# Kernel optimization log

Measured on AMD Instinct MI355X. Metric: run time of the kernel, lower is better.

## Reference

```python
import jax, jax.numpy as jnp
import numpy as np

N_NODES = 50000
N_EDGES = 1600000
N_GRAPHS = 256
IN_CH = 128
HID = 128
OUT_CH = 10


def gcn_conv(x, W, b, src, dst, ew, num_nodes):
    # PyG GCNConv: add self-loops (weight 1), symmetric deg^-1/2 normalization,
    # linear transform first, aggregate via scatter-add, bias after.
    loop = jnp.arange(num_nodes)
    s = jnp.concatenate([src, loop])
    d = jnp.concatenate([dst, loop])
    w = jnp.concatenate([ew, jnp.ones((num_nodes,), x.dtype)])
    deg = jax.ops.segment_sum(w, d, num_segments=num_nodes)
    dinv = jnp.where(deg > 0, jax.lax.rsqrt(deg), 0.0)
    norm = dinv[s] * dinv[d] * w                     # [E+N]
    h = x @ W                                        # [N, H]
    msg = h[s] * norm[:, None]                       # gather + scale
    out = jax.ops.segment_sum(msg, d, num_segments=num_nodes)  # scatter-add
    return out + b


def setup_inputs() -> dict:
    key = jax.random.key(0)
    ks = jax.random.split(key, 12)
    x = jax.random.normal(ks[0], (N_NODES, IN_CH), jnp.float32)
    edge_index = jax.random.randint(ks[1], (2, N_EDGES), 0, N_NODES, jnp.int64)
    edge_weight = jax.random.uniform(ks[2], (N_EDGES,), jnp.float32)
    batch = jnp.sort(jax.random.randint(ks[3], (N_NODES,), 0, N_GRAPHS, jnp.int64))
    s = 1.0 / np.sqrt(HID)
    W1 = jax.random.normal(ks[4], (IN_CH, HID), jnp.float32) / np.sqrt(IN_CH)
    b1 = jnp.zeros((HID,), jnp.float32)
    W2 = jax.random.normal(ks[5], (HID, HID), jnp.float32) * s
    b2 = jnp.zeros((HID,), jnp.float32)
    W3 = jax.random.normal(ks[6], (HID, HID), jnp.float32) * s
    b3 = jnp.zeros((HID,), jnp.float32)
    lw1 = jax.random.normal(ks[7], (HID, HID), jnp.float32) * s
    lb1 = jax.random.normal(ks[8], (HID,), jnp.float32) * s
    lw2 = jax.random.normal(ks[9], (HID, OUT_CH), jnp.float32) * s
    lb2 = jax.random.normal(ks[10], (OUT_CH,), jnp.float32) * s
    return {"x": x, "edge_index": edge_index, "edge_weight": edge_weight,
            "batch": batch, "W1": W1, "b1": b1, "W2": W2, "b2": b2,
            "W3": W3, "b3": b3, "lw1": lw1, "lb1": lb1, "lw2": lw2, "lb2": lb2}


def reference(x, edge_index, edge_weight, batch, W1, b1, W2, b2, W3, b3, lw1, lb1, lw2, lb2):
    src, dst = edge_index[0], edge_index[1]
    h = jax.nn.relu(gcn_conv(x, W1, b1, src, dst, edge_weight, N_NODES))
    h = jax.nn.relu(gcn_conv(h, W2, b2, src, dst, edge_weight, N_NODES))
    h = gcn_conv(h, W3, b3, src, dst, edge_weight, N_NODES)
    # global mean pool over graphs
    sums = jax.ops.segment_sum(h, batch, num_segments=N_GRAPHS)
    cnt = jax.ops.segment_sum(jnp.ones((N_NODES,), h.dtype), batch, num_segments=N_GRAPHS)
    emb = sums / jnp.maximum(cnt, 1.0)[:, None]      # [G, HID]
    out = (emb @ lw1 + lb1) @ lw2 + lb2              # classify: lin1 -> lin2
    return out
```

## Files before the change

### kernel.cpp

```cpp
#include <hip/hip_runtime.h>

#define N_NODES 50000
#define N_EDGES 1600000
#define N_GRAPHS 256
#define HID 128
#define OUT_CH 10
#define PAD 80
#define NBUCK 512
#define BNODES ((N_NODES + NBUCK - 1) / NBUCK)
#define BCAP 6144
#define P1BLK 256
#define EPB (N_EDGES / P1BLK)
#define DSENTINEL 127

typedef __bf16 bf16x8 __attribute__((ext_vector_type(8)));
typedef float f32x4 __attribute__((ext_vector_type(4)));

__device__ inline unsigned bf16rne(float f) {
    unsigned u = __float_as_uint(f);
    return (u + 0x7fffu + ((u >> 16) & 1u)) >> 16;
}

__global__ __launch_bounds__(1024) void bucket_k(const int* __restrict__ src,
                                                 const int* __restrict__ dst,
                                                 const float* __restrict__ ew,
                                                 int* __restrict__ bcount,
                                                 int2* __restrict__ cpair) {
    __shared__ int hist[NBUCK];
    __shared__ int base[NBUCK];
    int t = threadIdx.x;
    for (int i = t; i < NBUCK; i += 1024) hist[i] = 0;
    __syncthreads();
    int e0 = blockIdx.x * EPB;
    int e1 = e0 + EPB;
    for (int e = e0 + t; e < e1; e += 1024)
        atomicAdd(&hist[dst[e] / BNODES], 1);
    __syncthreads();
    for (int i = t; i < NBUCK; i += 1024) {
        int c = hist[i];
        base[i] = (c > 0) ? atomicAdd(&bcount[i], (c + 7) & ~7) : 0;
        hist[i] = 0;
    }
    __syncthreads();
    for (int e = e0 + t; e < e1; e += 1024) {
        int d = dst[e];
        int b = d / BNODES;
        int off = base[b] + atomicAdd(&hist[b], 1);
        if (off < BCAP) {
            int2 p;
            p.x = ((d - b * BNODES) << 16) | src[e];
            p.y = __float_as_int(ew[e]);
            cpair[b * BCAP + off] = p;
        }
    }
    __syncthreads();
    for (int i = t; i < NBUCK; i += 1024) {
        int c = hist[i];
        int ac = (c + 7) & ~7;
        for (int j = c; j < ac; ++j) {
            int off = base[i] + j;
            if (off < BCAP) {
                int2 p;
                p.x = DSENTINEL << 16;
                p.y = 0;
                cpair[i * BCAP + off] = p;
            }
        }
    }
}

__global__ __launch_bounds__(512) void ell_scatter_k(const int* __restrict__ bcount,
                                                     const int2* __restrict__ cpair,
                                                     int2* __restrict__ ell,
                                                     int* __restrict__ fill,
                                                     float* __restrict__ dinv) {
    __shared__ int lfill[BNODES];
    __shared__ float wsum[BNODES];
    int b = blockIdx.x;
    int t = threadIdx.x;
    for (int i = t; i < BNODES; i += 512) {
        lfill[i] = 0;
        wsum[i] = 0.f;
    }
    __syncthreads();
    int cnt = bcount[b];
    if (cnt > BCAP) cnt = BCAP;
    int n0 = b * BNODES;
    int sbase = b * BCAP;
    for (int i = t; i < cnt; i += 512) {
        int2 p = cpair[sbase + i];
        int dloc = p.x >> 16;
        if (dloc < BNODES) {
            int pos = atomicAdd(&lfill[dloc], 1);
            atomicAdd(&wsum[dloc], __int_as_float(p.y));
            if (pos < PAD) {
                int2 q;
                q.x = p.x & 0xffff;
                q.y = p.y;
                ell[(size_t)(n0 + dloc) * PAD + pos] = q;
            }
        }
    }
    __syncthreads();
    for (int i = t; i < BNODES; i += 512) {
        int n = n0 + i;
        if (n < N_NODES) {
            fill[n] = lfill[i] < PAD ? lfill[i] : PAD;
            dinv[n] = rsqrtf(wsum[i] + 1.0f);
        }
    }
}

__global__ __launch_bounds__(256) void scale_k(int2* __restrict__ ell,
                                               const int* __restrict__ fill,
                                               const float* __restrict__ dinv) {
    int idx = blockIdx.x * blockDim.x + threadIdx.x;
    if (idx >= N_NODES * PAD) return;
    int n = idx / PAD;
    int j = idx - n * PAD;
    if (j < fill[n]) {
        int2 p = ell[idx];
        p.y = __float_as_int(__int_as_float(p.y) * dinv[p.x] * dinv[n]);
        ell[idx] = p;
    }
}

__global__ void wprep_k(const float* __restrict__ W1, const float* __restrict__ W2,
                        const float* __restrict__ W3, unsigned short* __restrict__ Wt) {
    int idx = blockIdx.x * 256 + threadIdx.x;
    if (idx >= 3 * 16384) return;
    int m = idx >> 14;
    int r = idx & 16383;
    const float* W = (m == 0) ? W1 : (m == 1) ? W2 : W3;
    int c = r >> 7, k = r & 127;
    Wt[idx] = (unsigned short)bf16rne(W[k * 128 + c]);
}

__global__ __launch_bounds__(256) void gemm_mfma_k(const float* __restrict__ A32,
                                                   const unsigned short* __restrict__ Ab,
                                                   const unsigned short* __restrict__ Wt,
                                                   unsigned short* __restrict__ Cb,
                                                   int n_rows) {
    int tid = threadIdx.x;
    int wave = tid >> 6;
    int lane = tid & 63;
    int m = lane & 15;
    int quad = lane >> 4;
    int row = blockIdx.x * 64 + wave * 16 + m;
    int rowc = row < n_rows ? row : n_rows - 1;
    f32x4 acc[8] = {};
#pragma unroll
    for (int kc = 0; kc < 4; ++kc) {
        bf16x8 a;
        if (A32) {
            const float4* Ar = (const float4*)(A32 + (size_t)rowc * 128 + kc * 32 + quad * 8);
            float4 lo = Ar[0], hi = Ar[1];
            union { bf16x8 v; unsigned short s[8]; } u;
            u.s[0] = (unsigned short)bf16rne(lo.x);
            u.s[1] = (unsigned short)bf16rne(lo.y);
            u.s[2] = (unsigned short)bf16rne(lo.z);
            u.s[3] = (unsigned short)bf16rne(lo.w);
            u.s[4] = (unsigned short)bf16rne(hi.x);
            u.s[5] = (unsigned short)bf16rne(hi.y);
            u.s[6] = (unsigned short)bf16rne(hi.z);
            u.s[7] = (unsigned short)bf16rne(hi.w);
            a = u.v;
        } else {
            a = *(const bf16x8*)(Ab + (size_t)rowc * 128 + kc * 32 + quad * 8);
        }
#pragma unroll
        for (int ct = 0; ct < 8; ++ct) {
            bf16x8 b = *(const bf16x8*)(Wt + (size_t)(ct * 16 + m) * 128 + kc * 32 + quad * 8);
            acc[ct] = __builtin_amdgcn_mfma_f32_16x16x32_bf16(a, b, acc[ct], 0, 0, 0);
        }
    }
    int obase = blockIdx.x * 64 + wave * 16 + quad * 4;
#pragma unroll
    for (int ct = 0; ct < 8; ++ct) {
#pragma unroll
        for (int r = 0; r < 4; ++r) {
            int n = obase + r;
            if (n < n_rows)
                Cb[(size_t)n * 128 + ct * 16 + m] = (unsigned short)bf16rne(acc[ct][r]);
        }
    }
}

__global__ __launch_bounds__(256) void agg_k(const unsigned short* __restrict__ tb,
                                             const int* __restrict__ fill,
                                             const int2* __restrict__ ell,
                                             const float* __restrict__ dinv,
                                             const float* __restrict__ bias,
                                             unsigned short* __restrict__ outB, int relu) {
    int lane = threadIdx.x & 31;
    int local = threadIdx.x >> 5;
    int n = blockIdx.x * 8 + local;
    if (n >= N_NODES) return;
    float di = dinv[n];
    float sw = di * di;
#define BF4(q, f0, f1, f2, f3)                                    \
    float f0 = __uint_as_float((q).x << 16);                      \
    float f1 = __uint_as_float((q).x & 0xffff0000u);              \
    float f2 = __uint_as_float((q).y << 16);                      \
    float f3 = __uint_as_float((q).y & 0xffff0000u);
    uint2 qs = ((const uint2*)(tb + (size_t)n * 128))[lane];
    BF4(qs, sx, sy, sz, sw4)
    float4 acc = make_float4(sx * sw, sy * sw, sz * sw, sw4 * sw);
    const int2* ep = ell + n * PAD;
    int c = fill[n];
    int i = 0;
    for (; i + 8 <= c; i += 8) {
        int2 p0 = ep[i], p1 = ep[i + 1], p2 = ep[i + 2], p3 = ep[i + 3];
        int2 p4 = ep[i + 4], p5 = ep[i + 5], p6 = ep[i + 6], p7 = ep[i + 7];
        uint2 q0 = ((const uint2*)(tb + (size_t)p0.x * 128))[lane];
        uint2 q1 = ((const uint2*)(tb + (size_t)p1.x * 128))[lane];
        uint2 q2 = ((const uint2*)(tb + (size_t)p2.x * 128))[lane];
        uint2 q3 = ((const uint2*)(tb + (size_t)p3.x * 128))[lane];
        uint2 q4 = ((const uint2*)(tb + (size_t)p4.x * 128))[lane];
        uint2 q5 = ((const uint2*)(tb + (size_t)p5.x * 128))[lane];
        uint2 q6 = ((const uint2*)(tb + (size_t)p6.x * 128))[lane];
        uint2 q7 = ((const uint2*)(tb + (size_t)p7.x * 128))[lane];
        float w0 = __int_as_float(p0.y), w1 = __int_as_float(p1.y);
        float w2 = __int_as_float(p2.y), w3 = __int_as_float(p3.y);
        float w4 = __int_as_float(p4.y), w5 = __int_as_float(p5.y);
        float w6 = __int_as_float(p6.y), w7 = __int_as_float(p7.y);
        BF4(q0, a0, b0, c0, d0)
        BF4(q1, a1, b1, c1, d1)
        BF4(q2, a2, b2, c2, d2)
        BF4(q3, a3, b3, c3, d3)
        BF4(q4, a4, b4, c4, d4)
        BF4(q5, a5, b5, c5, d5)
        BF4(q6, a6, b6, c6, d6)
        BF4(q7, a7, b7, c7, d7)
        acc.x += a0 * w0 + a1 * w1 + a2 * w2 + a3 * w3 + a4 * w4 + a5 * w5 + a6 * w6 + a7 * w7;
        acc.y += b0 * w0 + b1 * w1 + b2 * w2 + b3 * w3 + b4 * w4 + b5 * w5 + b6 * w6 + b7 * w7;
        acc.z += c0 * w0 + c1 * w1 + c2 * w2 + c3 * w3 + c4 * w4 + c5 * w5 + c6 * w6 + c7 * w7;
        acc.w += d0 * w0 + d1 * w1 + d2 * w2 + d3 * w3 + d4 * w4 + d5 * w5 + d6 * w6 + d7 * w7;
    }
    for (; i + 4 <= c; i += 4) {
        int2 p0 = ep[i], p1 = ep[i + 1], p2 = ep[i + 2], p3 = ep[i + 3];
        float w0 = __int_as_float(p0.y), w1 = __int_as_float(p1.y);
        float w2 = __int_as_float(p2.y), w3 = __int_as_float(p3.y);
        uint2 q0 = ((const uint2*)(tb + (size_t)p0.x * 128))[lane];
        uint2 q1 = ((const uint2*)(tb + (size_t)p1.x * 128))[lane];
        uint2 q2 = ((const uint2*)(tb + (size_t)p2.x * 128))[lane];
        uint2 q3 = ((const uint2*)(tb + (size_t)p3.x * 128))[lane];
        BF4(q0, a0, b0, c0, d0)
        BF4(q1, a1, b1, c1, d1)
        BF4(q2, a2, b2, c2, d2)
        BF4(q3, a3, b3, c3, d3)
        acc.x += a0 * w0 + a1 * w1 + a2 * w2 + a3 * w3;
        acc.y += b0 * w0 + b1 * w1 + b2 * w2 + b3 * w3;
        acc.z += c0 * w0 + c1 * w1 + c2 * w2 + c3 * w3;
        acc.w += d0 * w0 + d1 * w1 + d2 * w2 + d3 * w3;
    }
    for (; i < c; ++i) {
        int2 p = ep[i];
        float w = __int_as_float(p.y);
        uint2 q = ((const uint2*)(tb + (size_t)p.x * 128))[lane];
        BF4(q, a0, b0, c0, d0)
        acc.x += a0 * w; acc.y += b0 * w; acc.z += c0 * w; acc.w += d0 * w;
    }
#undef BF4
    float4 b = ((const float4*)bias)[lane];
    acc.x += b.x; acc.y += b.y; acc.z += b.z; acc.w += b.w;
    if (relu) {
        acc.x = fmaxf(acc.x, 0.f);
        acc.y = fmaxf(acc.y, 0.f);
        acc.z = fmaxf(acc.z, 0.f);
        acc.w = fmaxf(acc.w, 0.f);
    }
    uint2 pk;
    pk.x = bf16rne(acc.x) | (bf16rne(acc.y) << 16);
    pk.y = bf16rne(acc.z) | (bf16rne(acc.w) << 16);
    ((uint2*)(outB + (size_t)n * 128))[lane] = pk;
}

__global__ void gbound_k(const int* __restrict__ batch, int* __restrict__ gstart) {
    int n = blockIdx.x * blockDim.x + threadIdx.x;
    if (n >= N_NODES) return;
    int b = batch[n];
    int bprev = (n == 0) ? -1 : batch[n - 1];
    for (int g = bprev + 1; g <= b; ++g) gstart[g] = n;
    if (n == N_NODES - 1) {
        for (int g = b + 1; g <= N_GRAPHS; ++g) gstart[g] = N_NODES;
    }
}

#define PCHUNK 49
__global__ __launch_bounds__(128) void pool1_k(const unsigned short* __restrict__ hb,
                                               const int* __restrict__ batch,
                                               float* __restrict__ pool) {
    int c = threadIdx.x;
    int n0 = blockIdx.x * PCHUNK;
    if (n0 >= N_NODES) return;
    int n1 = n0 + PCHUNK;
    if (n1 > N_NODES) n1 = N_NODES;
    int g = batch[n0];
    float run = 0.f;
    for (int n = n0; n < n1; ++n) {
        int gn = batch[n];
        if (gn != g) {
            atomicAdd(&pool[g * 128 + c], run);
            run = 0.f;
            g = gn;
        }
        run += __uint_as_float((unsigned)hb[(size_t)n * 128 + c] << 16);
    }
    atomicAdd(&pool[g * 128 + c], run);
}

__global__ __launch_bounds__(128) void cls2_k(const float* __restrict__ pool,
                                              const int* __restrict__ gstart,
                                              const float* __restrict__ lw1,
                                              const float* __restrict__ lb1,
                                              const float* __restrict__ lw2,
                                              const float* __restrict__ lb2,
                                              float* __restrict__ out) {
    __shared__ float emb[128];
    __shared__ float mid[128];
    int g = blockIdx.x, c = threadIdx.x;
    float cntf = fmaxf((float)(gstart[g + 1] - gstart[g]), 1.0f);
    emb[c] = pool[(size_t)g * 128 + c] / cntf;
    __syncthreads();
    float a = lb1[c];
    for (int k = 0; k < 128; ++k) a += emb[k] * lw1[k * 128 + c];
    mid[c] = a;
    __syncthreads();
    if (c < OUT_CH) {
        float o = lb2[c];
        for (int k = 0; k < 128; ++k) o += mid[k] * lw2[k * OUT_CH + c];
        out[g * OUT_CH + c] = o;
    }
}

extern "C" void kernel_launch(void* const* d_in, const int* in_sizes, int n_in,
                              void* d_out, int out_size, void* d_ws, size_t ws_size,
                              hipStream_t stream) {
    const float* x = (const float*)d_in[0];
    const int* ei = (const int*)d_in[1];
    const int* src = ei;
    const int* dst = ei + N_EDGES;
    const float* ew = (const float*)d_in[2];
    const int* batch = (const int*)d_in[3];
    const float* W1 = (const float*)d_in[4];
    const float* b1 = (const float*)d_in[5];
    const float* W2 = (const float*)d_in[6];
    const float* b2 = (const float*)d_in[7];
    const float* W3 = (const float*)d_in[8];
    const float* b3 = (const float*)d_in[9];
    const float* lw1 = (const float*)d_in[10];
    const float* lb1 = (const float*)d_in[11];
    const float* lw2 = (const float*)d_in[12];
    const float* lb2 = (const float*)d_in[13];
    float* out = (float*)d_out;

    char* ws = (char*)d_ws;
    size_t off = 0;
    auto alloc = [&](size_t bytes) {
        size_t cur = off;
        off += (bytes + 255) & ~(size_t)255;
        return cur;
    };
    size_t o_bcount = alloc(NBUCK * 4);
    size_t o_pool = alloc(N_GRAPHS * HID * 4);
    size_t zero_end = off;
    size_t o_fill = alloc(N_NODES * 4);
    size_t o_dinv = alloc(N_NODES * 4);
    size_t o_gstart = alloc((N_GRAPHS + 1) * 4);
    size_t o_wt = alloc(3 * 16384 * 2);
    size_t o_ell = alloc((size_t)N_NODES * PAD * 8);
    size_t o_cpair = alloc((size_t)NBUCK * BCAP * 8);
    size_t o_gAb = alloc((size_t)N_NODES * HID * 2);
    size_t o_aggB = alloc((size_t)N_NODES * HID * 2);
    (void)ws_size;

    int* bcount = (int*)(ws + o_bcount);
    float* pool = (float*)(ws + o_pool);
    int* fill = (int*)(ws + o_fill);
    float* dinv = (float*)(ws + o_dinv);
    int* gstart = (int*)(ws + o_gstart);
    unsigned short* Wt = (unsigned short*)(ws + o_wt);
    int2* ell = (int2*)(ws + o_ell);
    int2* cpair = (int2*)(ws + o_cpair);
    unsigned short* gAb = (unsigned short*)(ws + o_gAb);
    unsigned short* aggB = (unsigned short*)(ws + o_aggB);

    hipMemsetAsync(d_ws, 0, zero_end, stream);

    int nb = (N_NODES + 255) / 256;
    bucket_k<<<P1BLK, 1024, 0, stream>>>(src, dst, ew, bcount, cpair);
    ell_scatter_k<<<NBUCK, 512, 0, stream>>>(bcount, cpair, ell, fill, dinv);
    scale_k<<<(N_NODES * PAD + 255) / 256, 256, 0, stream>>>(ell, fill, dinv);
    gbound_k<<<nb, 256, 0, stream>>>(batch, gstart);
    wprep_k<<<192, 256, 0, stream>>>(W1, W2, W3, Wt);

    int gemm_blocks = (N_NODES + 63) / 64;
    int agg_blocks = (N_NODES + 7) / 8;
    gemm_mfma_k<<<gemm_blocks, 256, 0, stream>>>(x, (const unsigned short*)0, Wt, gAb, N_NODES);
    agg_k<<<agg_blocks, 256, 0, stream>>>(gAb, fill, ell, dinv, b1, aggB, 1);
    gemm_mfma_k<<<gemm_blocks, 256, 0, stream>>>((const float*)0, aggB, Wt + 16384, gAb, N_NODES);
    agg_k<<<agg_blocks, 256, 0, stream>>>(gAb, fill, ell, dinv, b2, aggB, 1);
    gemm_mfma_k<<<gemm_blocks, 256, 0, stream>>>((const float*)0, aggB, Wt + 32768, gAb, N_NODES);
    agg_k<<<agg_blocks, 256, 0, stream>>>(gAb, fill, ell, dinv, b3, aggB, 0);

    pool1_k<<<(N_NODES + PCHUNK - 1) / PCHUNK, 128, 0, stream>>>(aggB, batch, pool);
    cls2_k<<<N_GRAPHS, 128, 0, stream>>>(pool, gstart, lw1, lb1, lw2, lb2, out);
}
```

Baseline: 400.0 us.

## Widen aggregation gathers to 16 lanes per node, vectorize bucketing, fuse prep kernels

The aggregation kernel now gives each node 16 lanes, each loading a uint4 (8 bf16 features), instead of 32 lanes loading uint2. That doubles the nodes per block and reduces the number of memory instructions per gathered row. The bucketing kernel reads dst as int4 with 250 blocks so each block's edge range stays int4-aligned. The gbound and weight-prep kernels are merged into one launch. The aggregation unroll drops from 8 to 4 neighbors, which may reduce memory-level parallelism per thread.

```diff
diff --git a/kernel.cpp b/kernel.cpp
--- a/kernel.cpp
+++ b/kernel.cpp
@@ -9,7 +9,7 @@
 #define NBUCK 512
 #define BNODES ((N_NODES + NBUCK - 1) / NBUCK)
 #define BCAP 6144
-#define P1BLK 256
+#define P1BLK 250
 #define EPB (N_EDGES / P1BLK)
 #define DSENTINEL 127
 
@@ -31,10 +31,16 @@
     int t = threadIdx.x;
     for (int i = t; i < NBUCK; i += 1024) hist[i] = 0;
     __syncthreads();
-    int e0 = blockIdx.x * EPB;
-    int e1 = e0 + EPB;
-    for (int e = e0 + t; e < e1; e += 1024)
-        atomicAdd(&hist[dst[e] / BNODES], 1);
+    const int ch0 = blockIdx.x * (EPB / 4);
+    const int ch1 = ch0 + (EPB / 4);
+    const int4* dst4 = (const int4*)dst;
+    for (int ci = ch0 + t; ci < ch1; ci += 1024) {
+        int4 d4 = dst4[ci];
+        atomicAdd(&hist[d4.x / BNODES], 1);
+        atomicAdd(&hist[d4.y / BNODES], 1);
+        atomicAdd(&hist[d4.z / BNODES], 1);
+        atomicAdd(&hist[d4.w / BNODES], 1);
+    }
     __syncthreads();
     for (int i = t; i < NBUCK; i += 1024) {
         int c = hist[i];
@@ -42,16 +48,25 @@
         hist[i] = 0;
     }
     __syncthreads();
-    for (int e = e0 + t; e < e1; e += 1024) {
-        int d = dst[e];
-        int b = d / BNODES;
-        int off = base[b] + atomicAdd(&hist[b], 1);
-        if (off < BCAP) {
-            int2 p;
-            p.x = ((d - b * BNODES) << 16) | src[e];
-            p.y = __float_as_int(ew[e]);
-            cpair[b * BCAP + off] = p;
-        }
+    for (int ci = ch0 + t; ci < ch1; ci += 1024) {
+        int4 d4 = dst4[ci];
+        int e = ci * 4;
+#define PROC(dd, ee)                                              \
+        {                                                         \
+            int b = (dd) / BNODES;                                \
+            int off = base[b] + atomicAdd(&hist[b], 1);           \
+            if (off < BCAP) {                                     \
+                int2 p;                                           \
+                p.x = (((dd) - b * BNODES) << 16) | src[ee];      \
+                p.y = __float_as_int(ew[ee]);                     \
+                cpair[b * BCAP + off] = p;                        \
+            }                                                     \
+        }
+        PROC(d4.x, e)
+        PROC(d4.y, e + 1)
+        PROC(d4.z, e + 2)
+        PROC(d4.w, e + 3)
+#undef PROC
     }
     __syncthreads();
     for (int i = t; i < NBUCK; i += 1024) {
@@ -125,15 +140,28 @@
     }
 }
 
-__global__ void wprep_k(const float* __restrict__ W1, const float* __restrict__ W2,
-                        const float* __restrict__ W3, unsigned short* __restrict__ Wt) {
+__global__ __launch_bounds__(256) void prep_k(const int* __restrict__ batch,
+                                              int* __restrict__ gstart,
+                                              const float* __restrict__ W1,
+                                              const float* __restrict__ W2,
+                                              const float* __restrict__ W3,
+                                              unsigned short* __restrict__ Wt) {
     int idx = blockIdx.x * 256 + threadIdx.x;
-    if (idx >= 3 * 16384) return;
-    int m = idx >> 14;
-    int r = idx & 16383;
-    const float* W = (m == 0) ? W1 : (m == 1) ? W2 : W3;
-    int c = r >> 7, k = r & 127;
-    Wt[idx] = (unsigned short)bf16rne(W[k * 128 + c]);
+    if (idx < 3 * 16384) {
+        int m = idx >> 14;
+        int r = idx & 16383;
+        const float* W = (m == 0) ? W1 : (m == 1) ? W2 : W3;
+        int c = r >> 7, k = r & 127;
+        Wt[idx] = (unsigned short)bf16rne(W[k * 128 + c]);
+    }
+    if (idx < N_NODES) {
+        int b = batch[idx];
+        int bprev = (idx == 0) ? -1 : batch[idx - 1];
+        for (int g = bprev + 1; g <= b; ++g) gstart[g] = idx;
+        if (idx == N_NODES - 1) {
+            for (int g = b + 1; g <= N_GRAPHS; ++g) gstart[g] = N_NODES;
+        }
+    }
 }
 
 __global__ __launch_bounds__(256) void gemm_mfma_k(const float* __restrict__ A32,
@@ -192,99 +220,74 @@
                                              const float* __restrict__ dinv,
                                              const float* __restrict__ bias,
                                              unsigned short* __restrict__ outB, int relu) {
-    int lane = threadIdx.x & 31;
-    int local = threadIdx.x >> 5;
-    int n = blockIdx.x * 8 + local;
+    int lane = threadIdx.x & 15;
+    int local = threadIdx.x >> 4;
+    int n = blockIdx.x * 16 + local;
     if (n >= N_NODES) return;
     float di = dinv[n];
     float sw = di * di;
-#define BF4(q, f0, f1, f2, f3)                                    \
-    float f0 = __uint_as_float((q).x << 16);                      \
-    float f1 = __uint_as_float((q).x & 0xffff0000u);              \
-    float f2 = __uint_as_float((q).y << 16);                      \
-    float f3 = __uint_as_float((q).y & 0xffff0000u);
-    uint2 qs = ((const uint2*)(tb + (size_t)n * 128))[lane];
-    BF4(qs, sx, sy, sz, sw4)
-    float4 acc = make_float4(sx * sw, sy * sw, sz * sw, sw4 * sw);
+#define UNP(q, f)                                                 \
+    float f##0 = __uint_as_float((q).x << 16);                    \
+    float f##1 = __uint_as_float((q).x & 0xffff0000u);            \
+    float f##2 = __uint_as_float((q).y << 16);                    \
+    float f##3 = __uint_as_float((q).y & 0xffff0000u);            \
+    float f##4 = __uint_as_float((q).z << 16);                    \
+    float f##5 = __uint_as_float((q).z & 0xffff0000u);            \
+    float f##6 = __uint_as_float((q).w << 16);                    \
+    float f##7 = __uint_as_float((q).w & 0xffff0000u);
+    uint4 qs = ((const uint4*)(tb + (size_t)n * 128))[lane];
+    UNP(qs, s)
+    float acc0 = s0 * sw, acc1 = s1 * sw, acc2 = s2 * sw, acc3 = s3 * sw;
+    float acc4 = s4 * sw, acc5 = s5 * sw, acc6 = s6 * sw, acc7 = s7 * sw;
     const int2* ep = ell + n * PAD;
     int c = fill[n];
     int i = 0;
-    for (; i + 8 <= c; i += 8) {
+    for (; i + 4 <= c; i += 4) {
         int2 p0 = ep[i], p1 = ep[i + 1], p2 = ep[i + 2], p3 = ep[i + 3];
-        int2 p4 = ep[i + 4], p5 = ep[i + 5], p6 = ep[i + 6], p7 = ep[i + 7];
-        uint2 q0 = ((const uint2*)(tb + (size_t)p0.x * 128))[lane];
-        uint2 q1 = ((const uint2*)(tb + (size_t)p1.x * 128))[lane];
-        uint2 q2 = ((const uint2*)(tb + (size_t)p2.x * 128))[lane];
-        uint2 q3 = ((const uint2*)(tb + (size_t)p3.x * 128))[lane];
-        uint2 q4 = ((const uint2*)(tb + (size_t)p4.x * 128))[lane];
-        uint2 q5 = ((const uint2*)(tb + (size_t)p5.x * 128))[lane];
-        uint2 q6 = ((const uint2*)(tb + (size_t)p6.x * 128))[lane];
-        uint2 q7 = ((const uint2*)(tb + (size_t)p7.x * 128))[lane];
+        uint4 q0 = ((const uint4*)(tb + (size_t)p0.x * 128))[lane];
+        uint4 q1 = ((const uint4*)(tb + (size_t)p1.x * 128))[lane];
+        uint4 q2 = ((const uint4*)(tb + (size_t)p2.x * 128))[lane];
+        uint4 q3 = ((const uint4*)(tb + (size_t)p3.x * 128))[lane];
         float w0 = __int_as_float(p0.y), w1 = __int_as_float(p1.y);
         float w2 = __int_as_float(p2.y), w3 = __int_as_float(p3.y);
-        float w4 = __int_as_float(p4.y), w5 = __int_as_float(p5.y);
-        float w6 = __int_as_float(p6.y), w7 = __int_as_float(p7.y);
-        BF4(q0, a0, b0, c0, d0)
-        BF4(q1, a1, b1, c1, d1)
-        BF4(q2, a2, b2, c2, d2)
-        BF4(q3, a3, b3, c3, d3)
-        BF4(q4, a4, b4, c4, d4)
-        BF4(q5, a5, b5, c5, d5)
-        BF4(q6, a6, b6, c6, d6)
-        BF4(q7, a7, b7, c7, d7)
-        acc.x += a0 * w0 + a1 * w1 + a2 * w2 + a3 * w3 + a4 * w4 + a5 * w5 + a6 * w6 + a7 * w7;
-        acc.y += b0 * w0 + b1 * w1 + b2 * w2 + b3 * w3 + b4 * w4 + b5 * w5 + b6 * w6 + b7 * w7;
-        acc.z += c0 * w0 + c1 * w1 + c2 * w2 + c3 * w3 + c4 * w4 + c5 * w5 + c6 * w6 + c7 * w7;
-        acc.w += d0 * w0 + d1 * w1 + d2 * w2 + d3 * w3 + d4 * w4 + d5 * w5 + d6 * w6 + d7 * w7;
-    }
-    for (; i + 4 <= c; i += 4) {
-        int2 p0 = ep[i], p1 = ep[i + 1], p2 = ep[i + 2], p3 = ep[i + 3];
-        float w0 = __int_as_float(p0.y), w1 = __int_as_float(p1.y);
-        float w2 = __int_as_float(p2.y), w3 = __int_as_float(p3.y);
-        uint2 q0 = ((const uint2*)(tb + (size_t)p0.x * 128))[lane];
-        uint2 q1 = ((const uint2*)(tb + (size_t)p1.x * 128))[lane];
-        uint2 q2 = ((const uint2*)(tb + (size_t)p2.x * 128))[lane];
-        uint2 q3 = ((const uint2*)(tb + (size_t)p3.x * 128))[lane];
-        BF4(q0, a0, b0, c0, d0)
-        BF4(q1, a1, b1, c1, d1)
-        BF4(q2, a2, b2, c2, d2)
-        BF4(q3, a3, b3, c3, d3)
-        acc.x += a0 * w0 + a1 * w1 + a2 * w2 + a3 * w3;
-        acc.y += b0 * w0 + b1 * w1 + b2 * w2 + b3 * w3;
-        acc.z += c0 * w0 + c1 * w1 + c2 * w2 + c3 * w3;
-        acc.w += d0 * w0 + d1 * w1 + d2 * w2 + d3 * w3;
+        UNP(q0, a)
+        UNP(q1, b)
+        UNP(q2, cc)
+        UNP(q3, d)
+        acc0 += a0 * w0 + b0 * w1 + cc0 * w2 + d0 * w3;
+        acc1 += a1 * w0 + b1 * w1 + cc1 * w2 + d1 * w3;
+        acc2 += a2 * w0 + b2 * w1 + cc2 * w2 + d2 * w3;
+        acc3 += a3 * w0 + b3 * w1 + cc3 * w2 + d3 * w3;
+        acc4 += a4 * w0 + b4 * w1 + cc4 * w2 + d4 * w3;
+        acc5 += a5 * w0 + b5 * w1 + cc5 * w2 + d5 * w3;
+        acc6 += a6 * w0 + b6 * w1 + cc6 * w2 + d6 * w3;
+        acc7 += a7 * w0 + b7 * w1 + cc7 * w2 + d7 * w3;
     }
     for (; i < c; ++i) {
         int2 p = ep[i];
         float w = __int_as_float(p.y);
-        uint2 q = ((const uint2*)(tb + (size_t)p.x * 128))[lane];
-        BF4(q, a0, b0, c0, d0)
-        acc.x += a0 * w; acc.y += b0 * w; acc.z += c0 * w; acc.w += d0 * w;
-    }
-#undef BF4
-    float4 b = ((const float4*)bias)[lane];
-    acc.x += b.x; acc.y += b.y; acc.z += b.z; acc.w += b.w;
+        uint4 q = ((const uint4*)(tb + (size_t)p.x * 128))[lane];
+        UNP(q, a)
+        acc0 += a0 * w; acc1 += a1 * w; acc2 += a2 * w; acc3 += a3 * w;
+        acc4 += a4 * w; acc5 += a5 * w; acc6 += a6 * w; acc7 += a7 * w;
+    }
+#undef UNP
+    float4 b0 = ((const float4*)bias)[lane * 2];
+    float4 b1 = ((const float4*)bias)[lane * 2 + 1];
+    acc0 += b0.x; acc1 += b0.y; acc2 += b0.z; acc3 += b0.w;
+    acc4 += b1.x; acc5 += b1.y; acc6 += b1.z; acc7 += b1.w;
     if (relu) {
-        acc.x = fmaxf(acc.x, 0.f);
-        acc.y = fmaxf(acc.y, 0.f);
-        acc.z = fmaxf(acc.z, 0.f);
-        acc.w = fmaxf(acc.w, 0.f);
-    }
-    uint2 pk;
-    pk.x = bf16rne(acc.x) | (bf16rne(acc.y) << 16);
-    pk.y = bf16rne(acc.z) | (bf16rne(acc.w) << 16);
-    ((uint2*)(outB + (size_t)n * 128))[lane] = pk;
-}
-
-__global__ void gbound_k(const int* __restrict__ batch, int* __restrict__ gstart) {
-    int n = blockIdx.x * blockDim.x + threadIdx.x;
-    if (n >= N_NODES) return;
-    int b = batch[n];
-    int bprev = (n == 0) ? -1 : batch[n - 1];
-    for (int g = bprev + 1; g <= b; ++g) gstart[g] = n;
-    if (n == N_NODES - 1) {
-        for (int g = b + 1; g <= N_GRAPHS; ++g) gstart[g] = N_NODES;
-    }
+        acc0 = fmaxf(acc0, 0.f); acc1 = fmaxf(acc1, 0.f);
+        acc2 = fmaxf(acc2, 0.f); acc3 = fmaxf(acc3, 0.f);
+        acc4 = fmaxf(acc4, 0.f); acc5 = fmaxf(acc5, 0.f);
+        acc6 = fmaxf(acc6, 0.f); acc7 = fmaxf(acc7, 0.f);
+    }
+    uint4 pk;
+    pk.x = bf16rne(acc0) | (bf16rne(acc1) << 16);
+    pk.y = bf16rne(acc2) | (bf16rne(acc3) << 16);
+    pk.z = bf16rne(acc4) | (bf16rne(acc5) << 16);
+    pk.w = bf16rne(acc6) | (bf16rne(acc7) << 16);
+    ((uint4*)(outB + (size_t)n * 128))[lane] = pk;
 }
 
 #define PCHUNK 49
@@ -388,15 +391,13 @@
 
     hipMemsetAsync(d_ws, 0, zero_end, stream);
 
-    int nb = (N_NODES + 255) / 256;
     bucket_k<<<P1BLK, 1024, 0, stream>>>(src, dst, ew, bcount, cpair);
     ell_scatter_k<<<NBUCK, 512, 0, stream>>>(bcount, cpair, ell, fill, dinv);
     scale_k<<<(N_NODES * PAD + 255) / 256, 256, 0, stream>>>(ell, fill, dinv);
-    gbound_k<<<nb, 256, 0, stream>>>(batch, gstart);
-    wprep_k<<<192, 256, 0, stream>>>(W1, W2, W3, Wt);
+    prep_k<<<196, 256, 0, stream>>>(batch, gstart, W1, W2, W3, Wt);
 
     int gemm_blocks = (N_NODES + 63) / 64;
-    int agg_blocks = (N_NODES + 7) / 8;
+    int agg_blocks = (N_NODES + 15) / 16;
     gemm_mfma_k<<<gemm_blocks, 256, 0, stream>>>(x, (const unsigned short*)0, Wt, gAb, N_NODES);
     agg_k<<<agg_blocks, 256, 0, stream>>>(gAb, fill, ell, dinv, b1, aggB, 1);
     gemm_mfma_k<<<gemm_blocks, 256, 0, stream>>>((const float*)0, aggB, Wt + 16384, gAb, N_NODES);
```

Measured after the change: 402.5 us. No clear change (+0.6%).
